# Kernel tuning notes

Hardware: AMD Instinct MI355X
Metric: run time of the kernel (lower is better)

Reference implementation:

```python
import jax, jax.numpy as jnp
import numpy as np

B, T, D, K, NC, U = 64, 1024, 512, 5, 3, 256
BN_EPS = 1e-3  # keras BatchNormalization default epsilon


def setup_inputs() -> dict:
    key = jax.random.key(0)
    ks = jax.random.split(key, 8)
    return {
        "inputs": jax.random.normal(ks[0], (B, T, D), jnp.float32),
        "conv_kernels": jax.random.normal(ks[1], (NC, K, D, D), jnp.float32) * 0.02,
        "conv_biases": jnp.zeros((NC, D), jnp.float32),
        "bn_gamma": jnp.ones((NC, D), jnp.float32),
        "bn_beta": jnp.zeros((NC, D), jnp.float32),
        "bn_mean": jnp.zeros((NC, D), jnp.float32),
        "bn_var": jnp.ones((NC, D), jnp.float32),
        "lstm_kernel_fw": jax.random.normal(ks[2], (D, 4 * U), jnp.float32) * 0.04,
        "lstm_rec_fw": jax.random.normal(ks[3], (U, 4 * U), jnp.float32) * 0.04,
        "lstm_bias_fw": jnp.zeros((4 * U,), jnp.float32),
        "lstm_kernel_bw": jax.random.normal(ks[4], (D, 4 * U), jnp.float32) * 0.04,
        "lstm_rec_bw": jax.random.normal(ks[5], (U, 4 * U), jnp.float32) * 0.04,
        "lstm_bias_bw": jnp.zeros((4 * U,), jnp.float32),
    }


def _lstm(x_tbd, Wk, Wr, b):
    # x_tbd: [T, B, D]. Keras LSTM gate order: i, f, g(cell), o.
    units = Wr.shape[0]
    pre = jnp.einsum('tbd,dg->tbg', x_tbd, Wk) + b  # hoist input GEMM out of scan
    bsz = x_tbd.shape[1]

    def step(carry, p):
        h, c = carry
        z = p + h @ Wr
        i, f, g, o = jnp.split(z, 4, axis=-1)
        i = jax.nn.sigmoid(i)
        f = jax.nn.sigmoid(f)
        g = jnp.tanh(g)
        o = jax.nn.sigmoid(o)
        c = f * c + i * g
        h = o * jnp.tanh(c)
        return (h, c), h

    init = (jnp.zeros((bsz, units), x_tbd.dtype), jnp.zeros((bsz, units), x_tbd.dtype))
    _, hs = jax.lax.scan(step, init, pre)
    return hs  # [T, B, U]


def reference(inputs, conv_kernels, conv_biases, bn_gamma, bn_beta, bn_mean, bn_var,
              lstm_kernel_fw, lstm_rec_fw, lstm_bias_fw,
              lstm_kernel_bw, lstm_rec_bw, lstm_bias_bw):
    x = inputs  # [B, T, D]
    n_convs = conv_kernels.shape[0]
    for i in range(n_convs):
        x = jax.lax.conv_general_dilated(
            x, conv_kernels[i], window_strides=(1,), padding='SAME',
            dimension_numbers=('NWC', 'WIO', 'NWC')) + conv_biases[i]
        # BatchNorm, inference mode (moving stats), then ReLU
        x = bn_gamma[i] * (x - bn_mean[i]) * jax.lax.rsqrt(bn_var[i] + BN_EPS) + bn_beta[i]
        x = jax.nn.relu(x)
    xt = jnp.transpose(x, (1, 0, 2))  # [T, B, D]
    h_fw = _lstm(xt, lstm_kernel_fw, lstm_rec_fw, lstm_bias_fw)
    h_bw = _lstm(xt[::-1], lstm_kernel_bw, lstm_rec_bw, lstm_bias_bw)[::-1]
    out = jnp.concatenate([h_fw, h_bw], axis=-1)  # [T, B, 2U]
    return jnp.transpose(out, (1, 0, 2))  # [B, T, 2U]
```

## Files before the change

### kernel.cpp

```cpp
#include <hip/hip_runtime.h>

typedef _Float16 f16;
typedef _Float16 f16x8 __attribute__((ext_vector_type(8)));
typedef float f32x4 __attribute__((ext_vector_type(4)));
typedef unsigned long long u64;

#define BB 64
#define TT 1024
#define TP 1028
#define DD 512

static constexpr size_t SZ_XPAD = (size_t)BB * TP * DD * 2;
static constexpr size_t OFF_XA  = 0;
static constexpr size_t OFF_XB  = OFF_XA + SZ_XPAD;
static constexpr size_t OFF_KWA = OFF_XB + SZ_XPAD;
static constexpr size_t SZ_KWA  = (size_t)480 * 16384;
static constexpr size_t OFF_WKA = OFF_KWA + SZ_KWA;
static constexpr size_t SZ_WKA  = (size_t)128 * 16384;
static constexpr size_t OFF_WRA = OFF_WKA + SZ_WKA;
static constexpr size_t SZ_WRA  = (size_t)524288 * 2;
static constexpr size_t OFF_SCSH= OFF_WRA + SZ_WRA;
static constexpr size_t OFF_PRE = OFF_SCSH + 4096;
static constexpr size_t SZ_PRE  = (size_t)BB * TT * 2048 * 2;
static constexpr size_t OFF_HG  = OFF_PRE + SZ_PRE;
static constexpr size_t SZ_HG   = (size_t)16 * 8192;

__device__ __forceinline__ void gld16(const void* g, void* l) {
  __builtin_amdgcn_global_load_lds(
      (const __attribute__((address_space(1))) unsigned*)g,
      (__attribute__((address_space(3))) unsigned*)l, 16, 0, 0);
}

__device__ __forceinline__ float sigm(float x) {
  x = fminf(fmaxf(x, -30.f), 30.f);
  return 1.f / (1.f + __expf(-x));
}
__device__ __forceinline__ float tanh_(float x) {
  x = fminf(fmaxf(x, -15.f), 15.f);
  float e = __expf(2.f * x);
  return (e - 1.f) / (e + 1.f);
}

__global__ void prep_scale(const float* __restrict__ cb, const float* __restrict__ gm,
                           const float* __restrict__ bt, const float* __restrict__ mn,
                           const float* __restrict__ vr, float* __restrict__ scsh,
                           unsigned* __restrict__ hgw) {
  int i = blockIdx.x * 256 + threadIdx.x;
  hgw[i] = ((i >> 10) & 1) ? 0u : 0x00010001u;
  if (i < 3 * 512) {
    float rs = rsqrtf(vr[i] + 1e-3f);
    float s = gm[i] * rs;
    scsh[i] = s;
    scsh[1536 + i] = (cb[i] - mn[i]) * s + bt[i];
  }
}

__global__ void prep_x(const float* __restrict__ x, f16* __restrict__ xa, f16* __restrict__ xb) {
  size_t idx = (size_t)blockIdx.x * 256 + threadIdx.x;
  int d = (int)(idx & 511);
  int r = (int)(idx >> 9);
  int t2 = r % TP;
  int b = r / TP;
  int t = t2 - 2;
  bool in = (t >= 0 && t < TT);
  f16 v = in ? (f16)x[((size_t)b * TT + t) * DD + d] : (f16)0.f;
  xa[idx] = v;
  if (!in) xb[idx] = (f16)0.f;
}

__global__ void prep_convw(const float* __restrict__ ck, f16* __restrict__ kwa) {
  size_t idx = (size_t)blockIdx.x * 256 + threadIdx.x;
  int dout = (int)(idx & 511);
  int din = (int)((idx >> 9) & 511);
  int k5 = (int)((idx >> 18) % 5);
  int l = (int)(idx / ((size_t)5 << 18));
  f16 v = (f16)ck[idx];
  int blk = ((l * 5 + k5) * 4 + (dout >> 7)) * 8 + (din >> 6);
  int n = dout & 127, kk = din & 63;
  size_t dst = (size_t)blk * 8192 + (size_t)n * 64 + (size_t)(((kk >> 3) ^ (n & 7)) * 8) + (kk & 7);
  kwa[dst] = v;
}

__global__ void prep_wk(const float* __restrict__ wf, const float* __restrict__ wb2, f16* __restrict__ wka) {
  size_t idx = (size_t)blockIdx.x * 256 + threadIdx.x;
  int c = (int)(idx & 2047);
  int din = (int)(idx >> 11);
  float s = (c < 1024) ? wf[(size_t)din * 1024 + c] : wb2[(size_t)din * 1024 + (c - 1024)];
  int blk = (c >> 7) * 8 + (din >> 6);
  int n = c & 127, kk = din & 63;
  size_t dst = (size_t)blk * 8192 + (size_t)n * 64 + (size_t)(((kk >> 3) ^ (n & 7)) * 8) + (kk & 7);
  wka[dst] = (f16)s;
}

__global__ void prep_wr(const float* __restrict__ wf, const float* __restrict__ wb2, f16* __restrict__ wra) {
  size_t idx = (size_t)blockIdx.x * 256 + threadIdx.x;
  int c = (int)(idx & 1023);
  int k = (int)((idx >> 10) & 255);
  int dir = (int)(idx >> 18);
  float s = dir ? wb2[(size_t)k * 1024 + c] : wf[(size_t)k * 1024 + c];
  int gate = c >> 8;
  int u = c & 255;
  int ssub = u >> 4;
  int hf = ssub >> 3, w = ssub & 7;
  int l15 = u & 15;
  int ks = k >> 5, lhi = (k >> 3) & 3, j = k & 7;
  int lane = lhi * 16 + l15;
  size_t dst = ((((size_t)(dir * 2 + hf) * 8 + w) * 4 + gate) * 8 + ks) * 512 + (size_t)lane * 8 + j;
  wra[dst] = (f16)s;
}

__global__ __launch_bounds__(256, 3) void conv_gemm(
    const f16* __restrict__ xin, f16* __restrict__ xout,
    const f16* __restrict__ kwb, const float* __restrict__ scl, const float* __restrict__ shl) {
  __shared__ f16 Al[8192];
  __shared__ f16 Bl[8192];
  const int tid = threadIdx.x;
  const int lane = tid & 63;
  const int w = tid >> 6, wm = w >> 1, wn = w & 1;
  const int r15 = lane & 15, lhi = lane >> 4;
  const int wg = blockIdx.x;
  const int tm = wg >> 2, nb = wg & 3;
  const int b = tm >> 3, tblk = tm & 7;
  const size_t abase = (size_t)b * TP + (size_t)tblk * 128;

  int srow[4], asoff[4];
#pragma unroll
  for (int p = 0; p < 4; ++p) {
    int L = tid * 16 + p * 4096;
    int row = L >> 7, ch = (L >> 4) & 7;
    srow[p] = row;
    asoff[p] = (ch ^ (row & 7)) * 8;
  }

  f32x4 acc[4][4] = {};

  for (int k5 = 0; k5 < 5; ++k5) {
    for (int kb = 0; kb < 8; ++kb) {
#pragma unroll
      for (int p = 0; p < 4; ++p) {
        const f16* asrc = xin + (abase + (size_t)(k5 + srow[p])) * DD + kb * 64 + asoff[p];
        gld16(asrc, (char*)Al + tid * 16 + p * 4096);
      }
      const char* bbase = (const char*)kwb + (size_t)((k5 * 4 + nb) * 8 + kb) * 16384;
#pragma unroll
      for (int p = 0; p < 4; ++p)
        gld16(bbase + tid * 16 + p * 4096, (char*)Bl + tid * 16 + p * 4096);
      __syncthreads();
#pragma unroll
      for (int ks = 0; ks < 2; ++ks) {
        f16x8 af[4], bf[4];
#pragma unroll
        for (int m = 0; m < 4; ++m) {
          int row = wm * 64 + m * 16 + r15;
          int rc = (ks * 4 + lhi) ^ (row & 7);
          af[m] = *(const f16x8*)((const char*)Al + row * 128 + rc * 16);
        }
#pragma unroll
        for (int n = 0; n < 4; ++n) {
          int row = wn * 64 + n * 16 + r15;
          int rc = (ks * 4 + lhi) ^ (row & 7);
          bf[n] = *(const f16x8*)((const char*)Bl + row * 128 + rc * 16);
        }
#pragma unroll
        for (int m = 0; m < 4; ++m)
#pragma unroll
          for (int n = 0; n < 4; ++n)
            acc[m][n] = __builtin_amdgcn_mfma_f32_16x16x32_f16(af[m], bf[n], acc[m][n], 0, 0, 0);
      }
      __syncthreads();
    }
  }
#pragma unroll
  for (int n = 0; n < 4; ++n) {
    int c = nb * 128 + wn * 64 + n * 16 + r15;
    float s_ = scl[c], h_ = shl[c];
#pragma unroll
    for (int m = 0; m < 4; ++m) {
      int rl = wm * 64 + m * 16 + lhi * 4;
#pragma unroll
      for (int j = 0; j < 4; ++j) {
        float v = fmaxf(acc[m][n][j] * s_ + h_, 0.f);
        unsigned short us = __builtin_bit_cast(unsigned short, (f16)v);
        unsigned ot = (unsigned)__shfl_xor((int)us, 1, 64);
        if (!(lane & 1)) {
          unsigned pk = (unsigned)us | (ot << 16);
          *(unsigned*)((char*)xout + ((abase + 2 + rl + j) * DD + c) * 2) = pk;
        }
      }
    }
  }
}

__global__ __launch_bounds__(256, 3) void in_gemm(
    const f16* __restrict__ xin, f16* __restrict__ pre, const f16* __restrict__ wkb,
    const float* __restrict__ bfw, const float* __restrict__ bbw) {
  __shared__ f16 Al[8192];
  __shared__ f16 Bl[8192];
  const int tid = threadIdx.x;
  const int lane = tid & 63;
  const int w = tid >> 6, wm = w >> 1, wn = w & 1;
  const int r15 = lane & 15, lhi = lane >> 4;
  const int wg = blockIdx.x;
  const int tm = wg >> 4, nb = wg & 15;
  const int b = tm >> 3, tblk = tm & 7;
  const size_t abase = (size_t)b * TP + (size_t)tblk * 128 + 2;

  int srow[4], asoff[4];
#pragma unroll
  for (int p = 0; p < 4; ++p) {
    int L = tid * 16 + p * 4096;
    int row = L >> 7, ch = (L >> 4) & 7;
    srow[p] = row;
    asoff[p] = (ch ^ (row & 7)) * 8;
  }

  f32x4 acc[4][4] = {};

  for (int kb = 0; kb < 8; ++kb) {
#pragma unroll
    for (int p = 0; p < 4; ++p) {
      const f16* asrc = xin + (abase + (size_t)srow[p]) * DD + kb * 64 + asoff[p];
      gld16(asrc, (char*)Al + tid * 16 + p * 4096);
    }
    const char* bbase = (const char*)wkb + (size_t)(nb * 8 + kb) * 16384;
#pragma unroll
    for (int p = 0; p < 4; ++p)
      gld16(bbase + tid * 16 + p * 4096, (char*)Bl + tid * 16 + p * 4096);
    __syncthreads();
#pragma unroll
    for (int ks = 0; ks < 2; ++ks) {
      f16x8 af[4], bf[4];
#pragma unroll
      for (int m = 0; m < 4; ++m) {
        int row = wm * 64 + m * 16 + r15;
        int rc = (ks * 4 + lhi) ^ (row & 7);
        af[m] = *(const f16x8*)((const char*)Al + row * 128 + rc * 16);
      }
#pragma unroll
      for (int n = 0; n < 4; ++n) {
        int row = wn * 64 + n * 16 + r15;
        int rc = (ks * 4 + lhi) ^ (row & 7);
        bf[n] = *(const f16x8*)((const char*)Bl + row * 128 + rc * 16);
      }
#pragma unroll
      for (int m = 0; m < 4; ++m)
#pragma unroll
        for (int n = 0; n < 4; ++n)
          acc[m][n] = __builtin_amdgcn_mfma_f32_16x16x32_f16(af[m], bf[n], acc[m][n], 0, 0, 0);
    }
    __syncthreads();
  }
#pragma unroll
  for (int n = 0; n < 4; ++n) {
    int c = nb * 128 + wn * 64 + n * 16 + r15;
    float bias = (c < 1024) ? bfw[c] : bbw[c - 1024];
#pragma unroll
    for (int m = 0; m < 4; ++m) {
      int rl = wm * 64 + m * 16 + lhi * 4;
#pragma unroll
      for (int j = 0; j < 4; ++j) {
        float v = acc[m][n][j] + bias;
        unsigned short us = __builtin_bit_cast(unsigned short, (f16)v);
        unsigned ot = (unsigned)__shfl_xor((int)us, 1, 64);
        if (!(lane & 1)) {
          unsigned pk = (unsigned)us | (ot << 16);
          size_t prow = (size_t)b * TT + tblk * 128 + rl + j;
          *(unsigned*)((char*)pre + (prow * 2048 + c) * 2) = pk;
        }
      }
    }
  }
}

__global__ __launch_bounds__(512, 2) void lstm_rec(
    const f16* __restrict__ wra, const f16* __restrict__ pre, float* __restrict__ out,
    unsigned* __restrict__ hg) {
  __shared__ f16 hl[2][16 * 264];
  const int wg = blockIdx.x;
  const int dir = wg >> 3, bblk = (wg >> 1) & 3, half = wg & 1;
  const int ph = half ^ 1;
  const int pwg = wg ^ 1;
  const int tid = threadIdx.x;
  const int lane = tid & 63, w = tid >> 6;
  const int r15 = lane & 15, lhi = lane >> 4;
  const int ulocal = w * 16 + r15;
  const int u = half * 128 + ulocal;
  const int b0 = bblk * 16 + lhi * 4;

  f16x8 bfr[4][8];
  {
    const f16* wb0 = wra + (((size_t)(dir * 2 + half) * 8 + w) * 4) * 8 * 512;
#pragma unroll
    for (int g = 0; g < 4; ++g)
#pragma unroll
      for (int ks = 0; ks < 8; ++ks)
        bfr[g][ks] = *(const f16x8*)(wb0 + ((size_t)g * 8 + ks) * 512 + (size_t)lane * 8);
  }

  for (int i = tid; i < 2 * 16 * 264; i += 512) ((f16*)hl)[i] = (f16)0.f;
  __syncthreads();
  float cst[4] = {0.f, 0.f, 0.f, 0.f};
  const unsigned short* pr = (const unsigned short*)pre;
  const u64* pstage = (const u64*)((const char*)hg + (size_t)pwg * 8192);
  unsigned* myhg = (unsigned*)((char*)hg + (size_t)wg * 8192);
  const int srow = tid >> 5;
  const int schunk = tid & 31;

  for (int s = 0; s < TT; ++s) {
    const int t = dir ? (TT - 1 - s) : s;

    unsigned short pld[4][4];
#pragma unroll
    for (int g = 0; g < 4; ++g)
#pragma unroll
      for (int j = 0; j < 4; ++j)
        pld[g][j] = pr[((size_t)(b0 + j) * TT + t) * 2048 + dir * 1024 + g * 256 + u];

    if (s > 0) {
      const u64* pb = pstage + (size_t)(s & 1) * 512 + tid;
      const u64 expv = 0x0001000100010001ULL * (u64)(s & 3);
      u64 v8;
      do {
        v8 = __hip_atomic_load(pb, __ATOMIC_RELAXED, __HIP_MEMORY_SCOPE_AGENT);
      } while ((v8 & 0x0003000300030003ULL) != expv);
      *(u64*)((char*)hl[s & 1] + srow * 528 + ph * 256 + schunk * 8) = v8;
    }
    __syncthreads();

    f32x4 accv[4] = {};
    {
      const char* hb = (const char*)hl[s & 1];
#pragma unroll
      for (int ks = 0; ks < 8; ++ks) {
        f16x8 af = *(const f16x8*)(hb + r15 * 528 + ks * 64 + lhi * 16);
#pragma unroll
        for (int g = 0; g < 4; ++g)
          accv[g] = __builtin_amdgcn_mfma_f32_16x16x32_f16(af, bfr[g][ks], accv[g], 0, 0, 0);
      }
    }

    float hv[4];
#pragma unroll
    for (int j = 0; j < 4; ++j) {
      float zi = accv[0][j] + (float)__builtin_bit_cast(f16, pld[0][j]);
      float zf = accv[1][j] + (float)__builtin_bit_cast(f16, pld[1][j]);
      float zg = accv[2][j] + (float)__builtin_bit_cast(f16, pld[2][j]);
      float zo = accv[3][j] + (float)__builtin_bit_cast(f16, pld[3][j]);
      float ig = sigm(zi), fg = sigm(zf), gg = tanh_(zg), og = sigm(zo);
      float cc = fg * cst[j] + ig * gg;
      cst[j] = cc;
      hv[j] = og * tanh_(cc);
    }

    const unsigned tg2 = (unsigned)((s + 1) & 3);
    unsigned short t0 = (unsigned short)((__builtin_bit_cast(unsigned short, (f16)hv[0]) & 0xFFFCu) | tg2);
    unsigned short t1 = (unsigned short)((__builtin_bit_cast(unsigned short, (f16)hv[1]) & 0xFFFCu) | tg2);
    unsigned short t2 = (unsigned short)((__builtin_bit_cast(unsigned short, (f16)hv[2]) & 0xFFFCu) | tg2);
    unsigned short t3 = (unsigned short)((__builtin_bit_cast(unsigned short, (f16)hv[3]) & 0xFFFCu) | tg2);
    {
      unsigned o0 = (unsigned)__shfl_xor((int)t0, 1, 64);
      unsigned o1 = (unsigned)__shfl_xor((int)t1, 1, 64);
      unsigned o2 = (unsigned)__shfl_xor((int)t2, 1, 64);
      unsigned o3 = (unsigned)__shfl_xor((int)t3, 1, 64);
      if (!(lane & 1)) {
        unsigned* so = myhg + (size_t)((s + 1) & 1) * 1024 + (lhi * 4) * 64 + (ulocal >> 1);
        __hip_atomic_store(so,       (unsigned)t0 | (o0 << 16), __ATOMIC_RELAXED, __HIP_MEMORY_SCOPE_AGENT);
        __hip_atomic_store(so + 64,  (unsigned)t1 | (o1 << 16), __ATOMIC_RELAXED, __HIP_MEMORY_SCOPE_AGENT);
        __hip_atomic_store(so + 128, (unsigned)t2 | (o2 << 16), __ATOMIC_RELAXED, __HIP_MEMORY_SCOPE_AGENT);
        __hip_atomic_store(so + 192, (unsigned)t3 | (o3 << 16), __ATOMIC_RELAXED, __HIP_MEMORY_SCOPE_AGENT);
      }
    }

    {
      f16* hn = hl[(s + 1) & 1];
#pragma unroll
      for (int j = 0; j < 4; ++j)
        hn[(lhi * 4 + j) * 264 + half * 128 + ulocal] = (f16)hv[j];
    }
#pragma unroll
    for (int j = 0; j < 4; ++j)
      out[((size_t)(b0 + j) * TT + t) * DD + dir * 256 + u] = hv[j];
  }
}

extern "C" void kernel_launch(void* const* d_in, const int* in_sizes, int n_in,
                              void* d_out, int out_size, void* d_ws, size_t ws_size,
                              hipStream_t stream) {
  (void)in_sizes; (void)n_in; (void)out_size; (void)ws_size;
  char* ws = (char*)d_ws;
  f16* xa   = (f16*)(ws + OFF_XA);
  f16* xb   = (f16*)(ws + OFF_XB);
  f16* kwa  = (f16*)(ws + OFF_KWA);
  f16* wka  = (f16*)(ws + OFF_WKA);
  f16* wra  = (f16*)(ws + OFF_WRA);
  float* scsh = (float*)(ws + OFF_SCSH);
  f16* pre  = (f16*)(ws + OFF_PRE);
  unsigned* hg = (unsigned*)(ws + OFF_HG);

  const float* x   = (const float*)d_in[0];
  const float* ck  = (const float*)d_in[1];
  const float* cb  = (const float*)d_in[2];
  const float* gm  = (const float*)d_in[3];
  const float* bt  = (const float*)d_in[4];
  const float* mn  = (const float*)d_in[5];
  const float* vr  = (const float*)d_in[6];
  const float* wkf = (const float*)d_in[7];
  const float* wrf = (const float*)d_in[8];
  const float* bf  = (const float*)d_in[9];
  const float* wkb = (const float*)d_in[10];
  const float* wrb = (const float*)d_in[11];
  const float* bb2 = (const float*)d_in[12];

  prep_scale<<<128, 256, 0, stream>>>(cb, gm, bt, mn, vr, scsh, hg);
  prep_x<<<(BB * TP * DD) / 256, 256, 0, stream>>>(x, xa, xb);
  prep_convw<<<(3 * 5 * 512 * 512) / 256, 256, 0, stream>>>(ck, kwa);
  prep_wk<<<(512 * 2048) / 256, 256, 0, stream>>>(wkf, wkb, wka);
  prep_wr<<<(2 * 256 * 1024) / 256, 256, 0, stream>>>(wrf, wrb, wra);

  conv_gemm<<<2048, 256, 0, stream>>>(xa, xb, kwa,                  scsh,          scsh + 1536);
  conv_gemm<<<2048, 256, 0, stream>>>(xb, xa, kwa + 1 * 160 * 8192, scsh + 512,   scsh + 1536 + 512);
  conv_gemm<<<2048, 256, 0, stream>>>(xa, xb, kwa + 2 * 160 * 8192, scsh + 1024,  scsh + 1536 + 1024);

  in_gemm<<<8192, 256, 0, stream>>>(xb, pre, wka, bf, bb2);

  lstm_rec<<<16, 512, 0, stream>>>(wra, pre, (float*)d_out, hg);
}
```

Baseline: 3.999 ms.

## Merge LSTM half-pairs into single 1024-thread blocks, drop global spin sync

The recurrent LSTM kernel previously split the 256 hidden units across two 512-thread workgroups that exchanged h every step through tagged global-memory atomics and spin-waits. Now one 1024-thread workgroup owns all 256 units for a batch block, so h exchange goes only through double-buffered LDS with one barrier per step. The output store is deferred by a step and pointers are strength-reduced. Sigmoid and tanh drop input clamping and use hardware reciprocal. The cost is half as many workgroups (8 vs 16), lower parallelism, and 1024-thread occupancy pressure on registers holding the weight fragments.

Result: slower. 12.22 ms (+205.7%).

```diff
diff --git a/kernel.cpp b/kernel.cpp
--- a/kernel.cpp
+++ b/kernel.cpp
@@ -1,9 +1,9 @@
 #include <hip/hip_runtime.h>
+#include <type_traits>
 
 typedef _Float16 f16;
 typedef _Float16 f16x8 __attribute__((ext_vector_type(8)));
 typedef float f32x4 __attribute__((ext_vector_type(4)));
-typedef unsigned long long u64;
 
 #define BB 64
 #define TT 1024
@@ -22,8 +22,6 @@
 static constexpr size_t OFF_SCSH= OFF_WRA + SZ_WRA;
 static constexpr size_t OFF_PRE = OFF_SCSH + 4096;
 static constexpr size_t SZ_PRE  = (size_t)BB * TT * 2048 * 2;
-static constexpr size_t OFF_HG  = OFF_PRE + SZ_PRE;
-static constexpr size_t SZ_HG   = (size_t)16 * 8192;
 
 __device__ __forceinline__ void gld16(const void* g, void* l) {
   __builtin_amdgcn_global_load_lds(
@@ -32,21 +30,17 @@
 }
 
 __device__ __forceinline__ float sigm(float x) {
-  x = fminf(fmaxf(x, -30.f), 30.f);
-  return 1.f / (1.f + __expf(-x));
+  return __builtin_amdgcn_rcpf(1.f + __expf(-x));
 }
 __device__ __forceinline__ float tanh_(float x) {
-  x = fminf(fmaxf(x, -15.f), 15.f);
-  float e = __expf(2.f * x);
-  return (e - 1.f) / (e + 1.f);
+  float e = __expf(2.f * fminf(x, 15.f));
+  return (e - 1.f) * __builtin_amdgcn_rcpf(e + 1.f);
 }
 
 __global__ void prep_scale(const float* __restrict__ cb, const float* __restrict__ gm,
                            const float* __restrict__ bt, const float* __restrict__ mn,
-                           const float* __restrict__ vr, float* __restrict__ scsh,
-                           unsigned* __restrict__ hgw) {
+                           const float* __restrict__ vr, float* __restrict__ scsh) {
   int i = blockIdx.x * 256 + threadIdx.x;
-  hgw[i] = ((i >> 10) & 1) ? 0u : 0x00010001u;
   if (i < 3 * 512) {
     float rs = rsqrtf(vr[i] + 1e-3f);
     float s = gm[i] * rs;
@@ -100,12 +94,11 @@
   float s = dir ? wb2[(size_t)k * 1024 + c] : wf[(size_t)k * 1024 + c];
   int gate = c >> 8;
   int u = c & 255;
-  int ssub = u >> 4;
-  int hf = ssub >> 3, w = ssub & 7;
+  int wslot = u >> 4;
   int l15 = u & 15;
   int ks = k >> 5, lhi = (k >> 3) & 3, j = k & 7;
   int lane = lhi * 16 + l15;
-  size_t dst = ((((size_t)(dir * 2 + hf) * 8 + w) * 4 + gate) * 8 + ks) * 512 + (size_t)lane * 8 + j;
+  size_t dst = ((((size_t)(dir * 16 + wslot)) * 4 + gate) * 8 + ks) * 512 + (size_t)lane * 8 + j;
   wra[dst] = (f16)s;
 }
 
@@ -272,24 +265,20 @@
   }
 }
 
-__global__ __launch_bounds__(512, 2) void lstm_rec(
-    const f16* __restrict__ wra, const f16* __restrict__ pre, float* __restrict__ out,
-    unsigned* __restrict__ hg) {
+__global__ __launch_bounds__(1024, 1) void lstm_rec(
+    const f16* __restrict__ wra, const f16* __restrict__ pre, float* __restrict__ out) {
   __shared__ f16 hl[2][16 * 264];
   const int wg = blockIdx.x;
-  const int dir = wg >> 3, bblk = (wg >> 1) & 3, half = wg & 1;
-  const int ph = half ^ 1;
-  const int pwg = wg ^ 1;
+  const int dir = wg >> 2, bblk = wg & 3;
   const int tid = threadIdx.x;
-  const int lane = tid & 63, w = tid >> 6;
+  const int wv = tid >> 6, lane = tid & 63;
   const int r15 = lane & 15, lhi = lane >> 4;
-  const int ulocal = w * 16 + r15;
-  const int u = half * 128 + ulocal;
+  const int u = wv * 16 + r15;
   const int b0 = bblk * 16 + lhi * 4;
 
   f16x8 bfr[4][8];
   {
-    const f16* wb0 = wra + (((size_t)(dir * 2 + half) * 8 + w) * 4) * 8 * 512;
+    const f16* wb0 = wra + ((size_t)(dir * 16 + wv) * 4) * 8 * 512;
 #pragma unroll
     for (int g = 0; g < 4; ++g)
 #pragma unroll
@@ -297,49 +286,56 @@
         bfr[g][ks] = *(const f16x8*)(wb0 + ((size_t)g * 8 + ks) * 512 + (size_t)lane * 8);
   }
 
-  for (int i = tid; i < 2 * 16 * 264; i += 512) ((f16*)hl)[i] = (f16)0.f;
+  for (int i = tid; i < 2 * 16 * 264; i += 1024) ((f16*)hl)[i] = (f16)0.f;
   __syncthreads();
+
+  const unsigned short* pr16 = (const unsigned short*)pre;
+  const int t0 = dir ? (TT - 1) : 0;
+  const ptrdiff_t sPre = dir ? -2048 : 2048;
+  const ptrdiff_t sOut = dir ? -(ptrdiff_t)DD : DD;
+  const unsigned short* prp[4];
+  float* outp[4];
+#pragma unroll
+  for (int j = 0; j < 4; ++j) {
+    prp[j]  = pr16 + ((size_t)(b0 + j) * TT + t0) * 2048 + dir * 1024 + u;
+    outp[j] = out  + ((size_t)(b0 + j) * TT + t0) * DD   + dir * 256  + u;
+  }
+  const char* rdb = (const char*)hl + r15 * 528 + lhi * 16;
+  f16* wrb = (f16*)((char*)hl + (lhi * 4) * 528 + u * 2);
+
   float cst[4] = {0.f, 0.f, 0.f, 0.f};
-  const unsigned short* pr = (const unsigned short*)pre;
-  const u64* pstage = (const u64*)((const char*)hg + (size_t)pwg * 8192);
-  unsigned* myhg = (unsigned*)((char*)hg + (size_t)wg * 8192);
-  const int srow = tid >> 5;
-  const int schunk = tid & 31;
-
-  for (int s = 0; s < TT; ++s) {
-    const int t = dir ? (TT - 1 - s) : s;
+  float hvP[4] = {0.f, 0.f, 0.f, 0.f};
+
+  auto stepf = [&](int s, auto parc) {
+    constexpr int PAR = decltype(parc)::value;
+    constexpr int NPAR = PAR ^ 1;
+
+    if (s > 0) {
+#pragma unroll
+      for (int j = 0; j < 4; ++j) {
+        *outp[j] = hvP[j];
+        outp[j] += sOut;
+      }
+    }
 
     unsigned short pld[4][4];
 #pragma unroll
     for (int g = 0; g < 4; ++g)
 #pragma unroll
       for (int j = 0; j < 4; ++j)
-        pld[g][j] = pr[((size_t)(b0 + j) * TT + t) * 2048 + dir * 1024 + g * 256 + u];
-
-    if (s > 0) {
-      const u64* pb = pstage + (size_t)(s & 1) * 512 + tid;
-      const u64 expv = 0x0001000100010001ULL * (u64)(s & 3);
-      u64 v8;
-      do {
-        v8 = __hip_atomic_load(pb, __ATOMIC_RELAXED, __HIP_MEMORY_SCOPE_AGENT);
-      } while ((v8 & 0x0003000300030003ULL) != expv);
-      *(u64*)((char*)hl[s & 1] + srow * 528 + ph * 256 + schunk * 8) = v8;
-    }
-    __syncthreads();
+        pld[g][j] = prp[j][g * 256];
+#pragma unroll
+    for (int j = 0; j < 4; ++j) prp[j] += sPre;
 
     f32x4 accv[4] = {};
-    {
-      const char* hb = (const char*)hl[s & 1];
-#pragma unroll
-      for (int ks = 0; ks < 8; ++ks) {
-        f16x8 af = *(const f16x8*)(hb + r15 * 528 + ks * 64 + lhi * 16);
-#pragma unroll
-        for (int g = 0; g < 4; ++g)
-          accv[g] = __builtin_amdgcn_mfma_f32_16x16x32_f16(af, bfr[g][ks], accv[g], 0, 0, 0);
-      }
-    }
-
-    float hv[4];
+#pragma unroll
+    for (int ks = 0; ks < 8; ++ks) {
+      f16x8 af = *(const f16x8*)(rdb + PAR * 8448 + ks * 64);
+#pragma unroll
+      for (int g = 0; g < 4; ++g)
+        accv[g] = __builtin_amdgcn_mfma_f32_16x16x32_f16(af, bfr[g][ks], accv[g], 0, 0, 0);
+    }
+
 #pragma unroll
     for (int j = 0; j < 4; ++j) {
       float zi = accv[0][j] + (float)__builtin_bit_cast(f16, pld[0][j]);
@@ -349,38 +345,19 @@
       float ig = sigm(zi), fg = sigm(zf), gg = tanh_(zg), og = sigm(zo);
       float cc = fg * cst[j] + ig * gg;
       cst[j] = cc;
-      hv[j] = og * tanh_(cc);
-    }
-
-    const unsigned tg2 = (unsigned)((s + 1) & 3);
-    unsigned short t0 = (unsigned short)((__builtin_bit_cast(unsigned short, (f16)hv[0]) & 0xFFFCu) | tg2);
-    unsigned short t1 = (unsigned short)((__builtin_bit_cast(unsigned short, (f16)hv[1]) & 0xFFFCu) | tg2);
-    unsigned short t2 = (unsigned short)((__builtin_bit_cast(unsigned short, (f16)hv[2]) & 0xFFFCu) | tg2);
-    unsigned short t3 = (unsigned short)((__builtin_bit_cast(unsigned short, (f16)hv[3]) & 0xFFFCu) | tg2);
-    {
-      unsigned o0 = (unsigned)__shfl_xor((int)t0, 1, 64);
-      unsigned o1 = (unsigned)__shfl_xor((int)t1, 1, 64);
-      unsigned o2 = (unsigned)__shfl_xor((int)t2, 1, 64);
-      unsigned o3 = (unsigned)__shfl_xor((int)t3, 1, 64);
-      if (!(lane & 1)) {
-        unsigned* so = myhg + (size_t)((s + 1) & 1) * 1024 + (lhi * 4) * 64 + (ulocal >> 1);
-        __hip_atomic_store(so,       (unsigned)t0 | (o0 << 16), __ATOMIC_RELAXED, __HIP_MEMORY_SCOPE_AGENT);
-        __hip_atomic_store(so + 64,  (unsigned)t1 | (o1 << 16), __ATOMIC_RELAXED, __HIP_MEMORY_SCOPE_AGENT);
-        __hip_atomic_store(so + 128, (unsigned)t2 | (o2 << 16), __ATOMIC_RELAXED, __HIP_MEMORY_SCOPE_AGENT);
-        __hip_atomic_store(so + 192, (unsigned)t3 | (o3 << 16), __ATOMIC_RELAXED, __HIP_MEMORY_SCOPE_AGENT);
-      }
-    }
-
-    {
-      f16* hn = hl[(s + 1) & 1];
-#pragma unroll
-      for (int j = 0; j < 4; ++j)
-        hn[(lhi * 4 + j) * 264 + half * 128 + ulocal] = (f16)hv[j];
-    }
-#pragma unroll
-    for (int j = 0; j < 4; ++j)
-      out[((size_t)(b0 + j) * TT + t) * DD + dir * 256 + u] = hv[j];
-  }
+      float hv = og * tanh_(cc);
+      hvP[j] = hv;
+      wrb[j * 264 + NPAR * 4224] = (f16)hv;
+    }
+    __syncthreads();
+  };
+
+  for (int s = 0; s < TT; s += 2) {
+    stepf(s,     std::integral_constant<int, 0>{});
+    stepf(s + 1, std::integral_constant<int, 1>{});
+  }
+#pragma unroll
+  for (int j = 0; j < 4; ++j) *outp[j] = hvP[j];
 }
 
 extern "C" void kernel_launch(void* const* d_in, const int* in_sizes, int n_in,
@@ -395,7 +372,6 @@
   f16* wra  = (f16*)(ws + OFF_WRA);
   float* scsh = (float*)(ws + OFF_SCSH);
   f16* pre  = (f16*)(ws + OFF_PRE);
-  unsigned* hg = (unsigned*)(ws + OFF_HG);
 
   const float* x   = (const float*)d_in[0];
   const float* ck  = (const float*)d_in[1];
@@ -408,14 +384,14 @@
   const float* wrf = (const float*)d_in[8];
   const float* bf  = (const float*)d_in[9];
   const float* wkb = (const float*)d_in[10];
-  const float* wrb = (const float*)d_in[11];
+  const float* wrb2= (const float*)d_in[11];
   const float* bb2 = (const float*)d_in[12];
 
-  prep_scale<<<128, 256, 0, stream>>>(cb, gm, bt, mn, vr, scsh, hg);
+  prep_scale<<<6, 256, 0, stream>>>(cb, gm, bt, mn, vr, scsh);
   prep_x<<<(BB * TP * DD) / 256, 256, 0, stream>>>(x, xa, xb);
   prep_convw<<<(3 * 5 * 512 * 512) / 256, 256, 0, stream>>>(ck, kwa);
   prep_wk<<<(512 * 2048) / 256, 256, 0, stream>>>(wkf, wkb, wka);
-  prep_wr<<<(2 * 256 * 1024) / 256, 256, 0, stream>>>(wrf, wrb, wra);
+  prep_wr<<<(2 * 256 * 1024) / 256, 256, 0, stream>>>(wrf, wrb2, wra);
 
   conv_gemm<<<2048, 256, 0, stream>>>(xa, xb, kwa,                  scsh,          scsh + 1536);
   conv_gemm<<<2048, 256, 0, stream>>>(xb, xa, kwa + 1 * 160 * 8192, scsh + 512,   scsh + 1536 + 512);
@@ -423,5 +399,5 @@
 
   in_gemm<<<8192, 256, 0, stream>>>(xb, pre, wka, bf, bb2);
 
-  lstm_rec<<<16, 512, 0, stream>>>(wra, pre, (float*)d_out, hg);
-}
+  lstm_rec<<<8, 1024, 0, stream>>>(wra, pre, (float*)d_out);
+}
```
